# Kernel optimization log

Measured on AMD Instinct MI355X. Metric: run time of the kernel, lower is better.

Reference implementation:

```python
import jax, jax.numpy as jnp
import numpy as np

B, T, P = 8192, 1024, 12  # series, timesteps, seasonal_period
INIT_ALPHA = 0.5 / P


def setup_inputs() -> dict:
    key = jax.random.key(0)
    k1, k2, k3, k4 = jax.random.split(key, 4)
    # positive data/states to keep multiplicative-season divisions well-conditioned
    y = jax.random.uniform(k1, (B, T, 1), dtype=jnp.float32) + 0.5
    l0 = jax.random.uniform(k2, (B, 1), dtype=jnp.float32) + 0.5
    b0 = jax.random.uniform(k3, (B, 1), dtype=jnp.float32) * 0.1
    s0 = jax.random.uniform(k4, (B, P), dtype=jnp.float32) + 0.5
    # learned smoothing params, shape (input_dim=1, 1) as in build()
    alpha = jnp.full((1, 1), INIT_ALPHA, dtype=jnp.float32)
    beta = jnp.full((1, 1), 0.1 * INIT_ALPHA, dtype=jnp.float32)
    phi = jnp.full((1, 1), 0.99, dtype=jnp.float32)
    gamma = jnp.full((1, 1), 0.05 * INIT_ALPHA, dtype=jnp.float32)
    return {"y": y, "l0": l0, "b0": b0, "s0": s0,
            "alpha": alpha, "beta": beta, "phi": phi, "gamma": gamma}


def reference(y, l0, b0, s0, alpha, beta, phi, gamma):
    # Holt-Winters ES recurrence: additive trend, multiplicative season.
    def step(carry, yt):  # yt: [B,1]
        l_prev, b_prev, s_prev = carry
        l = alpha * yt / s_prev[:, :1] + (1.0 - alpha) * (l_prev + phi * b_prev)
        b = beta * (l - l_prev) + (1.0 - beta) * b_prev * phi
        c = gamma * yt / l + (1.0 - gamma) * s_prev[:, :1]
        s = jnp.concatenate([s_prev[:, 1:], c], axis=1)  # rotate seasonal buffer
        out = (l + b * phi) * s[:, :1]
        return (l, b, s), out

    ys = jnp.swapaxes(y, 0, 1)  # [T,B,1]
    _, outs = jax.lax.scan(step, (l0, b0, s0), ys)
    return jnp.swapaxes(outs, 0, 1)  # [B,T,1]
```

## Files before the change

### kernel.cpp

```cpp
#include <hip/hip_runtime.h>


#define LSY 65
#define YBW (64 * LSY)
#define LSO 65
#define OBW (64 * LSO)

typedef __attribute__((address_space(1))) const void* as1cv;
typedef __attribute__((address_space(3))) void* as3v;

template<int R>
__device__ __forceinline__ void batch16(
    const float* yb, float* ob, int base,
    float& l, float& bt, float& pn, float& rl, float* s, float* rs,
    float alpha, float oma, float beta, float nbeta, float ombphi,
    float gamma, float omg, float phi)
{
    float yv[16];
#pragma unroll
    for (int i = 0; i < 16; ++i) yv[i] = yb[base + i];

    float ov[16];
#pragma unroll
    for (int i = 0; i < 16; ++i) {
        const int J  = (R + i) % 12;
        const int Jn = (R + i + 1) % 12;
        const float yt = yv[i];
        const float ay = alpha * yt;
        const float a  = ay * rs[J];
        const float ln = fmaf(oma, pn, a);
        const float inner = fmaf(nbeta, l, ombphi * bt);
        const float bn  = fmaf(beta, ln, inner);
        const float pnn = fmaf(phi, bn, ln);
        rl = rl * fmaf(-ln, rl, 2.0f);
        const float gy = gamma * yt;
        const float c  = fmaf(gy, rl, omg * s[J]);
        s[J] = c;
        rs[J] = rs[J] * fmaf(-c, rs[J], 2.0f);
        ov[i] = pnn * s[Jn];
        l = ln; bt = bn; pn = pnn;
    }

#pragma unroll
    for (int i = 0; i < 16; ++i) ob[(base + i) * LSO] = ov[i];
}

#define BATCH_ARGS l, bt, pn, rl, s, rs, alpha, oma, beta, nbeta, ombphi, gamma, omg, phi

__global__ __launch_bounds__(256) void esrnn_kernel(
    const float* __restrict__ y, const float* __restrict__ l0,
    const float* __restrict__ b0, const float* __restrict__ s0,
    const float* __restrict__ alpha_p, const float* __restrict__ beta_p,
    const float* __restrict__ phi_p, const float* __restrict__ gamma_p,
    float* __restrict__ out)
{
    __shared__ float ybuf[2 * YBW];
    __shared__ float obuf[2 * OBW];

    const int tid  = threadIdx.x;
    const int wid  = tid >> 6;
    const int lane = tid & 63;

    const float alpha = alpha_p[0];
    const float beta  = beta_p[0];
    const float phi   = phi_p[0];
    const float gamma = gamma_p[0];
    const float oma    = 1.0f - alpha;
    const float omg    = 1.0f - gamma;
    const float nbeta  = -beta;
    const float ombphi = (1.0f - beta) * phi;

    const float* yg = y + (size_t)blockIdx.x * 64 * 1024;

    float l = 1.0f, bt = 0.0f, pn = 1.0f, rl = 1.0f;
    float s[12], rs[12];
#pragma unroll
    for (int k = 0; k < 12; ++k) { s[k] = 1.0f; rs[k] = 1.0f; }

    if (wid == 0) {
        const int b = blockIdx.x * 64 + lane;
        l  = l0[b];
        bt = b0[b];
        const float4 s03 = *(const float4*)(s0 + b * 12);
        const float4 s47 = *(const float4*)(s0 + b * 12 + 4);
        const float4 s8b = *(const float4*)(s0 + b * 12 + 8);
        s[0] = s03.x; s[1] = s03.y; s[2]  = s03.z; s[3]  = s03.w;
        s[4] = s47.x; s[5] = s47.y; s[6]  = s47.z; s[7]  = s47.w;
        s[8] = s8b.x; s[9] = s8b.y; s[10] = s8b.z; s[11] = s8b.w;
#pragma unroll
        for (int k = 0; k < 12; ++k) rs[k] = __builtin_amdgcn_rcpf(s[k]);
        rl = __builtin_amdgcn_rcpf(l);
        pn = fmaf(phi, bt, l);
    }

    for (int n = 0; n < 18; ++n) {
        if (wid == 1) {
            if (n <= 15) {
                const float* g = yg + n * 64 + lane;
                float* dst = ybuf + (size_t)(n & 1) * YBW;
#pragma unroll
                for (int r = 0; r < 64; ++r) {
                    __builtin_amdgcn_global_load_lds((as1cv)(g + r * 1024),
                                                     (as3v)(dst + r * LSY),
                                                     4, 0, 0);
                }
            }
        } else if (wid == 0) {
            if (n >= 1 && n <= 16) {
                const int c = n - 1;
                const float* yb = ybuf + (size_t)(c & 1) * YBW + lane * LSY;
                float*       ob = obuf + (size_t)(c & 1) * OBW + lane;
                const int m = c % 3;
                if (m == 0) {
                    batch16<0>(yb, ob, 0,  BATCH_ARGS);
                    batch16<4>(yb, ob, 16, BATCH_ARGS);
                    batch16<8>(yb, ob, 32, BATCH_ARGS);
                    batch16<0>(yb, ob, 48, BATCH_ARGS);
                } else if (m == 1) {
                    batch16<4>(yb, ob, 0,  BATCH_ARGS);
                    batch16<8>(yb, ob, 16, BATCH_ARGS);
                    batch16<0>(yb, ob, 32, BATCH_ARGS);
                    batch16<4>(yb, ob, 48, BATCH_ARGS);
                } else {
                    batch16<8>(yb, ob, 0,  BATCH_ARGS);
                    batch16<0>(yb, ob, 16, BATCH_ARGS);
                    batch16<4>(yb, ob, 32, BATCH_ARGS);
                    batch16<8>(yb, ob, 48, BATCH_ARGS);
                }
            }
        } else {
            if (n >= 2) {
                const int c = n - 2;
                const int sbase = (wid - 2) * 32;
                const float* obr = obuf + (size_t)(c & 1) * OBW + lane * LSO + sbase;
                float* og = out + (size_t)(blockIdx.x * 64 + sbase) * 1024
                                + c * 64 + lane;
#pragma unroll
                for (int r = 0; r < 32; ++r) {
                    og[(size_t)r * 1024] = obr[r];
                }
            }
        }
        __syncthreads();
    }
}

extern "C" void kernel_launch(void* const* d_in, const int* in_sizes, int n_in,
                              void* d_out, int out_size, void* d_ws, size_t ws_size,
                              hipStream_t stream) {
    const float* y     = (const float*)d_in[0];
    const float* l0    = (const float*)d_in[1];
    const float* b0    = (const float*)d_in[2];
    const float* s0    = (const float*)d_in[3];
    const float* alpha = (const float*)d_in[4];
    const float* beta  = (const float*)d_in[5];
    const float* phi   = (const float*)d_in[6];
    const float* gamma = (const float*)d_in[7];
    float* out = (float*)d_out;

    esrnn_kernel<<<dim3(128), dim3(256), 0, stream>>>(
        y, l0, b0, s0, alpha, beta, phi, gamma, out);
}
```

Measured before the change: 121.0 us.

## Halve series per block to 32 and launch 256 blocks with vectorized LDS access

Each block now handles 32 series instead of 64, so the grid doubles to 256 blocks and spreads the sequential recurrence over more compute units. Only half the lanes of the compute wavefront do work. The LDS strides change (68 and 36) so the y reads and output reads can use float4 loads instead of scalar LDS accesses. The cost is idle lanes in wave 0 and in the loader wave, in exchange for more CUs working at once on the latency-bound serial chain.

```diff
diff --git a/kernel.cpp b/kernel.cpp
--- a/kernel.cpp
+++ b/kernel.cpp
@@ -1,9 +1,10 @@
 #include <hip/hip_runtime.h>
 
 
-#define LSY 65
-#define YBW (64 * LSY)
-#define LSO 65
+#define NS  32
+#define LSY 68
+#define YBW (NS * LSY)
+#define LSO 36
 #define OBW (64 * LSO)
 
 typedef __attribute__((address_space(1))) const void* as1cv;
@@ -16,10 +17,12 @@
     float alpha, float oma, float beta, float nbeta, float ombphi,
     float gamma, float omg, float phi)
 {
-    float yv[16];
-#pragma unroll
-    for (int i = 0; i < 16; ++i) yv[i] = yb[base + i];
-
+    const float4 q0 = *(const float4*)(yb + base + 0);
+    const float4 q1 = *(const float4*)(yb + base + 4);
+    const float4 q2 = *(const float4*)(yb + base + 8);
+    const float4 q3 = *(const float4*)(yb + base + 12);
+    const float yv[16] = {q0.x, q0.y, q0.z, q0.w, q1.x, q1.y, q1.z, q1.w,
+                          q2.x, q2.y, q2.z, q2.w, q3.x, q3.y, q3.z, q3.w};
     float ov[16];
 #pragma unroll
     for (int i = 0; i < 16; ++i) {
@@ -40,7 +43,6 @@
         ov[i] = pnn * s[Jn];
         l = ln; bt = bn; pn = pnn;
     }
-
 #pragma unroll
     for (int i = 0; i < 16; ++i) ob[(base + i) * LSO] = ov[i];
 }
@@ -70,15 +72,15 @@
     const float nbeta  = -beta;
     const float ombphi = (1.0f - beta) * phi;
 
-    const float* yg = y + (size_t)blockIdx.x * 64 * 1024;
+    const float* yg = y + (size_t)blockIdx.x * NS * 1024;
 
     float l = 1.0f, bt = 0.0f, pn = 1.0f, rl = 1.0f;
     float s[12], rs[12];
 #pragma unroll
     for (int k = 0; k < 12; ++k) { s[k] = 1.0f; rs[k] = 1.0f; }
 
-    if (wid == 0) {
-        const int b = blockIdx.x * 64 + lane;
+    if (wid == 0 && lane < NS) {
+        const int b = blockIdx.x * NS + lane;
         l  = l0[b];
         bt = b0[b];
         const float4 s03 = *(const float4*)(s0 + b * 12);
@@ -99,14 +101,14 @@
                 const float* g = yg + n * 64 + lane;
                 float* dst = ybuf + (size_t)(n & 1) * YBW;
 #pragma unroll
-                for (int r = 0; r < 64; ++r) {
+                for (int r = 0; r < NS; ++r) {
                     __builtin_amdgcn_global_load_lds((as1cv)(g + r * 1024),
                                                      (as3v)(dst + r * LSY),
                                                      4, 0, 0);
                 }
             }
         } else if (wid == 0) {
-            if (n >= 1 && n <= 16) {
+            if (lane < NS && n >= 1 && n <= 16) {
                 const int c = n - 1;
                 const float* yb = ybuf + (size_t)(c & 1) * YBW + lane * LSY;
                 float*       ob = obuf + (size_t)(c & 1) * OBW + lane;
@@ -131,14 +133,23 @@
         } else {
             if (n >= 2) {
                 const int c = n - 2;
-                const int sbase = (wid - 2) * 32;
-                const float* obr = obuf + (size_t)(c & 1) * OBW + lane * LSO + sbase;
-                float* og = out + (size_t)(blockIdx.x * 64 + sbase) * 1024
+                const int sbase = (wid - 2) * 16;
+                const float* obr = obuf + (size_t)(c & 1) * OBW
+                                 + lane * LSO + sbase;
+                float* og = out + (size_t)(blockIdx.x * NS + sbase) * 1024
                                 + c * 64 + lane;
-#pragma unroll
-                for (int r = 0; r < 32; ++r) {
-                    og[(size_t)r * 1024] = obr[r];
-                }
+                float4 t0 = *(const float4*)(obr + 0);
+                float4 t1 = *(const float4*)(obr + 4);
+                float4 t2 = *(const float4*)(obr + 8);
+                float4 t3 = *(const float4*)(obr + 12);
+                og[ 0 * 1024] = t0.x; og[ 1 * 1024] = t0.y;
+                og[ 2 * 1024] = t0.z; og[ 3 * 1024] = t0.w;
+                og[ 4 * 1024] = t1.x; og[ 5 * 1024] = t1.y;
+                og[ 6 * 1024] = t1.z; og[ 7 * 1024] = t1.w;
+                og[ 8 * 1024] = t2.x; og[ 9 * 1024] = t2.y;
+                og[10 * 1024] = t2.z; og[11 * 1024] = t2.w;
+                og[12 * 1024] = t3.x; og[13 * 1024] = t3.y;
+                og[14 * 1024] = t3.z; og[15 * 1024] = t3.w;
             }
         }
         __syncthreads();
@@ -158,6 +169,6 @@
     const float* gamma = (const float*)d_in[7];
     float* out = (float*)d_out;
 
-    esrnn_kernel<<<dim3(128), dim3(256), 0, stream>>>(
+    esrnn_kernel<<<dim3(256), dim3(256), 0, stream>>>(
         y, l0, b0, s0, alpha, beta, phi, gamma, out);
 }
```

Result: slower. 126.3 us (+4.4%).
